# Optimization experiments

Hardware: AMD Instinct MI355X
Metric: run time of the kernel (lower is better)

## Reference

```python
import jax, jax.numpy as jnp
import numpy as np

LT_INDICES = np.array([[0, 1, 3], [1, 2, 4], [3, 4, 5]])  # lower-triangle -> 3x3
SYMEIG_EPS = 1e-6  # noise scale used by SymEig
N_GRADS = 64
B_VALUE = 1000.0


def _design_matrix(n_grads=N_GRADS, b=B_VALUE, seed=0):
    """dipy.reconst.dti.design_matrix equivalent: columns Dxx,Dxy,Dyy,Dxz,Dyz,Dzz, dummy; returns -B."""
    rng = np.random.default_rng(seed)
    g = rng.normal(size=(n_grads, 3))
    g /= np.linalg.norm(g, axis=1, keepdims=True)
    B = np.empty((n_grads, 7), dtype=np.float64)
    B[:, 0] = g[:, 0] * g[:, 0] * b
    B[:, 1] = g[:, 0] * g[:, 1] * 2.0 * b
    B[:, 2] = g[:, 1] * g[:, 1] * b
    B[:, 3] = g[:, 0] * g[:, 2] * 2.0 * b
    B[:, 4] = g[:, 1] * g[:, 2] * 2.0 * b
    B[:, 5] = g[:, 2] * g[:, 2] * b
    B[:, 6] = 1.0
    return -B


def setup_inputs() -> dict:
    key = jax.random.key(0)
    k1, _ = jax.random.split(key)
    D = _design_matrix()
    design_matrix_inv = jnp.asarray(np.linalg.pinv(D), dtype=jnp.float32)  # [7, n_grads]
    min_diffusivity = jnp.asarray(1e-6 / -D.min(), dtype=jnp.float32)
    dwi = jax.random.uniform(k1, (100, 100, 100, N_GRADS), dtype=jnp.float32)
    mask = jnp.ones((100, 100, 100, 1), dtype=jnp.float32)
    return {"dwi": dwi, "mask": mask, "design_matrix_inv": design_matrix_inv,
            "min_diffusivity": min_diffusivity}


def reference(dwi, mask, design_matrix_inv, min_diffusivity):
    # WLS log-linear DTI fit
    dwi = jnp.maximum(dwi, min_diffusivity)
    fit = jnp.einsum('ij,...j->...i', design_matrix_inv, jnp.log(dwi))  # [...,7]
    tensors = fit[..., LT_INDICES]  # [...,3,3] symmetric diffusion tensors
    # SymEig: add tiny gaussian noise (degeneracy breaking), re-symmetrize
    noise = SYMEIG_EPS * jax.random.normal(jax.random.key(42), tensors.shape, dtype=tensors.dtype)
    t = tensors + noise
    t = (t + jnp.swapaxes(t, -1, -2)) * 0.5
    eigenvals, eigenvectors = jnp.linalg.eigh(t)  # [...,3], [...,3,3]
    eigenvals = jnp.maximum(eigenvals, min_diffusivity)
    eigenvals = jnp.where(jnp.isnan(eigenvals), 0.0, eigenvals)
    all_zero = jnp.all(eigenvals == 0, axis=-1).astype(eigenvals.dtype)
    ev1, ev2, ev3 = eigenvals[..., 0], eigenvals[..., 1], eigenvals[..., 2]
    num = 0.5 * ((ev1 - ev2) ** 2 + (ev2 - ev3) ** 2 + (ev3 - ev1) ** 2)
    den = jnp.sum(eigenvals * eigenvals, axis=-1) + all_zero
    fa = jnp.sqrt(num / den)[..., None]  # [...,1]
    return fa * mask
```

## Files before the change

### kernel.cpp

```cpp
#include <hip/hip_runtime.h>


__device__ __forceinline__ unsigned tf_rotl(unsigned x, int r) {
  return (x << r) | (x >> (32 - r));
}

__device__ __forceinline__ unsigned threefry_second(unsigned x0, unsigned x1) {
  const unsigned k0 = 0u, k1 = 42u;
  const unsigned k2 = 0x1BD11BDAu ^ k0 ^ k1;
  x0 += k0; x1 += k1;
#define TF_ROUND(r) { x0 += x1; x1 = tf_rotl(x1, r); x1 ^= x0; }
  TF_ROUND(13) TF_ROUND(15) TF_ROUND(26) TF_ROUND(6)
  x0 += k1; x1 += k2 + 1u;
  TF_ROUND(17) TF_ROUND(29) TF_ROUND(16) TF_ROUND(24)
  x0 += k2; x1 += k0 + 2u;
  TF_ROUND(13) TF_ROUND(15) TF_ROUND(26) TF_ROUND(6)
  x0 += k0; x1 += k1 + 3u;
  TF_ROUND(17) TF_ROUND(29) TF_ROUND(16) TF_ROUND(24)
  x0 += k1; x1 += k2 + 4u;
  TF_ROUND(13) TF_ROUND(15) TF_ROUND(26) TF_ROUND(6)
  x0 += k2; x1 += k0 + 5u;
#undef TF_ROUND
  (void)x0;
  return x1;
}

__device__ __forceinline__ float erfinv_xla(float x) {
  float w = -__logf(fmaf(-x, x, 1.0f));
  float p;
  if (w < 5.0f) {
    w = w - 2.5f;
    p = 2.81022636e-08f;
    p = fmaf(p, w, 3.43273939e-07f);
    p = fmaf(p, w, -3.5233877e-06f);
    p = fmaf(p, w, -4.39150654e-06f);
    p = fmaf(p, w, 0.00021858087f);
    p = fmaf(p, w, -0.00125372503f);
    p = fmaf(p, w, -0.00417768164f);
    p = fmaf(p, w, 0.246640727f);
    p = fmaf(p, w, 1.50140941f);
  } else {
    w = __builtin_sqrtf(w) - 3.0f;
    p = -0.000200214257f;
    p = fmaf(p, w, 0.000100950558f);
    p = fmaf(p, w, 0.00134934322f);
    p = fmaf(p, w, -0.00367342844f);
    p = fmaf(p, w, 0.00573950773f);
    p = fmaf(p, w, -0.0076224613f);
    p = fmaf(p, w, 0.00943887047f);
    p = fmaf(p, w, 1.00167406f);
    p = fmaf(p, w, 2.83297682f);
  }
  return p * x;
}

__device__ __forceinline__ float jax_normal_at(unsigned idx) {
  unsigned bits = threefry_second(0u, idx);
  float f = __uint_as_float((bits >> 9) | 0x3F800000u);
  float u = f - 1.0f;
  const float lo = -0.99999994f;
  float val = fmaf(u, 2.0f, lo);
  val = fmaxf(lo, val);
  return 1.41421356237f * erfinv_xla(val);
}

#define NG 64

__global__ __launch_bounds__(256) void fa_kernel(
    const float* __restrict__ dwi,
    const float* __restrict__ mask,
    const float* __restrict__ W,
    const float* __restrict__ mdp,
    float* __restrict__ out,
    int nvox)
{
  int v = blockIdx.x * 256 + threadIdx.x;
  if (v >= nvox) return;
  const float md = mdp[0];

  const float4* __restrict__ p =
      reinterpret_cast<const float4*>(dwi + (size_t)v * NG);
  float f0 = 0.f, f1 = 0.f, f2 = 0.f, f3 = 0.f, f4 = 0.f, f5 = 0.f;
#pragma unroll
  for (int j4 = 0; j4 < NG / 4; ++j4) {
    float4 d = p[j4];
    float xs[4];
    xs[0] = __logf(fmaxf(d.x, md));
    xs[1] = __logf(fmaxf(d.y, md));
    xs[2] = __logf(fmaxf(d.z, md));
    xs[3] = __logf(fmaxf(d.w, md));
#pragma unroll
    for (int k = 0; k < 4; ++k) {
      int j = j4 * 4 + k;
      float x = xs[k];
      f0 = fmaf(W[0 * NG + j], x, f0);
      f1 = fmaf(W[1 * NG + j], x, f1);
      f2 = fmaf(W[2 * NG + j], x, f2);
      f3 = fmaf(W[3 * NG + j], x, f3);
      f4 = fmaf(W[4 * NG + j], x, f4);
      f5 = fmaf(W[5 * NG + j], x, f5);
    }
  }

  unsigned base = 9u * (unsigned)v;
  float z[9];
#pragma unroll
  for (int e = 0; e < 9; ++e) z[e] = jax_normal_at(base + (unsigned)e);

  const float eps = 1e-6f;
  float a00 = f0 + eps * z[0];
  float a11 = f2 + eps * z[4];
  float a22 = f5 + eps * z[8];
  float a01 = ((f1 + eps * z[1]) + (f1 + eps * z[3])) * 0.5f;
  float a02 = ((f3 + eps * z[2]) + (f3 + eps * z[6])) * 0.5f;
  float a12 = ((f4 + eps * z[5]) + (f4 + eps * z[7])) * 0.5f;

  float q = (a00 + a11 + a22) * (1.0f / 3.0f);
  float aa = a00 - q, bb = a11 - q, cc = a22 - q;
  float p2 = aa * aa + bb * bb + cc * cc +
             2.0f * (a01 * a01 + a02 * a02 + a12 * a12);
  float pp = __builtin_sqrtf(p2 * (1.0f / 6.0f));
  float invp = (pp > 0.0f) ? (1.0f / pp) : 0.0f;
  float b00 = aa * invp, b11 = bb * invp, b22 = cc * invp;
  float b01 = a01 * invp, b02 = a02 * invp, b12 = a12 * invp;
  float detB = b00 * (b11 * b22 - b12 * b12)
             - b01 * (b01 * b22 - b12 * b02)
             + b02 * (b01 * b12 - b11 * b02);
  float r = 0.5f * detB;
  r = fminf(1.0f, fmaxf(-1.0f, r));
  float phi = acosf(r) * (1.0f / 3.0f);
  float l0 = q + 2.0f * pp * cosf(phi);
  float l2 = q + 2.0f * pp * cosf(phi + 2.0943951023931953f);
  float l1 = 3.0f * q - l0 - l2;

  l0 = fmaxf(l0, md);
  l1 = fmaxf(l1, md);
  l2 = fmaxf(l2, md);
  float d01 = l0 - l1, d12 = l1 - l2, d20 = l2 - l0;
  float num = 0.5f * (d01 * d01 + d12 * d12 + d20 * d20);
  float den = l0 * l0 + l1 * l1 + l2 * l2;
  float fa = __builtin_sqrtf(num / den);

  out[v] = fa * mask[v];
}

extern "C" void kernel_launch(void* const* d_in, const int* in_sizes, int n_in,
                              void* d_out, int out_size, void* d_ws, size_t ws_size,
                              hipStream_t stream) {
  const float* dwi  = (const float*)d_in[0];
  const float* mask = (const float*)d_in[1];
  const float* W    = (const float*)d_in[2];
  const float* mdp  = (const float*)d_in[3];
  float* out = (float*)d_out;
  int nvox = in_sizes[0] / NG;
  int grid = (nvox + 255) / 256;
  hipLaunchKernelGGL(fa_kernel, dim3(grid), dim3(256), 0, stream,
                     dwi, mask, W, mdp, out, nvox);
}
```

Before: 357.8 us.

## Stage DWI tile into LDS via global_load_lds with XOR swizzle

Each block now copies its 256 voxels' gradient data into shared memory with coalesced direct global-to-LDS loads. The source slots are XOR-swizzled so that each thread's per-voxel float4 reads from LDS avoid bank conflicts. Previously every thread read its own contiguous 256-byte row with strided float4 loads, which coalesced poorly across the wavefront. The change uses 64 KB of LDS per block, which may limit occupancy, and adds a block-wide barrier before compute.

```diff
diff --git a/kernel.cpp b/kernel.cpp
--- a/kernel.cpp
+++ b/kernel.cpp
@@ -1,4 +1,5 @@
 #include <hip/hip_runtime.h>
+#include <stdint.h>
 
 
 __device__ __forceinline__ unsigned tf_rotl(unsigned x, int r) {
@@ -65,6 +66,10 @@
 }
 
 #define NG 64
+#define VPB 256
+
+typedef __attribute__((address_space(1))) const void gvoid_t;
+typedef __attribute__((address_space(3))) void lvoid_t;
 
 __global__ __launch_bounds__(256) void fa_kernel(
     const float* __restrict__ dwi,
@@ -74,16 +79,40 @@
     float* __restrict__ out,
     int nvox)
 {
-  int v = blockIdx.x * 256 + threadIdx.x;
+  __shared__ float4 smem[VPB * NG / 4];
+
+  const int t    = threadIdx.x;
+  const int wid  = t >> 6;
+  const int lane = t & 63;
+
+  const size_t blockBaseF = (size_t)blockIdx.x * VPB * NG;
+  const float* gbase = dwi + blockBaseF;
+  const size_t validSlots = ((size_t)nvox * NG - blockBaseF) >> 2;
+
+#pragma unroll
+  for (int i = 0; i < 16; ++i) {
+    const int baseSlot = wid * 1024 + i * 64;
+    const int slot = baseSlot + lane;
+    int srcSlot = slot ^ ((slot >> 4) & 7);
+    if ((size_t)srcSlot >= validSlots) srcSlot = 0;
+    __builtin_amdgcn_global_load_lds(
+        (gvoid_t*)(gbase + (size_t)srcSlot * 4),
+        (lvoid_t*)(smem + baseSlot),
+        16, 0, 0);
+  }
+  __syncthreads();
+
+  const int v = blockIdx.x * VPB + t;
   if (v >= nvox) return;
+
   const float md = mdp[0];
 
-  const float4* __restrict__ p =
-      reinterpret_cast<const float4*>(dwi + (size_t)v * NG);
+  const int rb = t << 4;
+  const int sw = t & 7;
   float f0 = 0.f, f1 = 0.f, f2 = 0.f, f3 = 0.f, f4 = 0.f, f5 = 0.f;
 #pragma unroll
-  for (int j4 = 0; j4 < NG / 4; ++j4) {
-    float4 d = p[j4];
+  for (int j4 = 0; j4 < 16; ++j4) {
+    float4 d = smem[rb + (j4 ^ sw)];
     float xs[4];
     xs[0] = __logf(fmaxf(d.x, md));
     xs[1] = __logf(fmaxf(d.y, md));
@@ -153,7 +182,7 @@
   const float* mdp  = (const float*)d_in[3];
   float* out = (float*)d_out;
   int nvox = in_sizes[0] / NG;
-  int grid = (nvox + 255) / 256;
-  hipLaunchKernelGGL(fa_kernel, dim3(grid), dim3(256), 0, stream,
+  int grid = (nvox + VPB - 1) / VPB;
+  hipLaunchKernelGGL(fa_kernel, dim3(grid), dim3(VPB), 0, stream,
                      dwi, mask, W, mdp, out, nvox);
 }
```

Result: slower. 372.6 us (+4.1%).

## Stage DWI through LDS with async global_load_lds double buffering

Applied to the files above, without the earlier changes.

Replaces per-thread strided float4 loads of each voxel's 64 gradients with wave-cooperative global_load_lds transfers into a swizzled, double-buffered shared-memory tile. The loads are issued ahead of the threefry noise generation so memory latency overlaps that compute, and later chunks are prefetched while earlier ones are consumed. The goal is coalesced global access in place of 256-byte-strided per-thread reads, plus overlap of load latency. It depends on manual vmcnt waits and an XOR swizzle being exactly right, adds 32KB of LDS per block, and sets launch_bounds to 4 blocks.

```diff
diff --git a/kernel.cpp b/kernel.cpp
--- a/kernel.cpp
+++ b/kernel.cpp
@@ -1,4 +1,5 @@
 #include <hip/hip_runtime.h>
+#include <stdint.h>
 
 
 __device__ __forceinline__ unsigned tf_rotl(unsigned x, int r) {
@@ -66,7 +67,13 @@
 
 #define NG 64
 
-__global__ __launch_bounds__(256) void fa_kernel(
+typedef __attribute__((address_space(1))) const void gvoid_t;
+typedef __attribute__((address_space(3))) void lvoid_t;
+
+#define VMWAIT(n) asm volatile("s_waitcnt vmcnt(" #n ")" ::: "memory")
+#define CLOB()    asm volatile("" ::: "memory")
+
+__global__ __launch_bounds__(256, 4) void fa_kernel(
     const float* __restrict__ dwi,
     const float* __restrict__ mask,
     const float* __restrict__ W,
@@ -74,38 +81,78 @@
     float* __restrict__ out,
     int nvox)
 {
-  int v = blockIdx.x * 256 + threadIdx.x;
-  if (v >= nvox) return;
+  __shared__ float4 smem[4][2][256];
+
+  const int t    = threadIdx.x;
+  const int wid  = t >> 6;
+  const int lane = t & 63;
+  const int v    = blockIdx.x * 256 + t;
+  const size_t wvox    = (size_t)blockIdx.x * 256 + (size_t)(wid * 64);
+  const size_t totalF4 = (size_t)nvox * (NG / 4);
+
   const float md = mdp[0];
 
-  const float4* __restrict__ p =
-      reinterpret_cast<const float4*>(dwi + (size_t)v * NG);
+#define STAGE(c, b) do {                                                   \
+    _Pragma("unroll")                                                      \
+    for (int i = 0; i < 4; ++i) {                                          \
+      int vl = i * 16 + (lane >> 2);                                       \
+      int q  = (lane & 3) ^ ((vl >> 1) & 3);                               \
+      size_t src = (wvox + (size_t)vl) * (NG / 4) + (c) * 4 + (size_t)q;   \
+      if (src >= totalF4) src = 0;            \
+      __builtin_amdgcn_global_load_lds(                                    \
+          (gvoid_t*)(dwi + src * 4),                                       \
+          (lvoid_t*)(&smem[wid][(b)][i * 64]), 16, 0, 0);                  \
+    }                                                                      \
+    CLOB();                                                                \
+  } while (0)
+
   float f0 = 0.f, f1 = 0.f, f2 = 0.f, f3 = 0.f, f4 = 0.f, f5 = 0.f;
-#pragma unroll
-  for (int j4 = 0; j4 < NG / 4; ++j4) {
-    float4 d = p[j4];
-    float xs[4];
-    xs[0] = __logf(fmaxf(d.x, md));
-    xs[1] = __logf(fmaxf(d.y, md));
-    xs[2] = __logf(fmaxf(d.z, md));
-    xs[3] = __logf(fmaxf(d.w, md));
-#pragma unroll
-    for (int k = 0; k < 4; ++k) {
-      int j = j4 * 4 + k;
-      float x = xs[k];
-      f0 = fmaf(W[0 * NG + j], x, f0);
-      f1 = fmaf(W[1 * NG + j], x, f1);
-      f2 = fmaf(W[2 * NG + j], x, f2);
-      f3 = fmaf(W[3 * NG + j], x, f3);
-      f4 = fmaf(W[4 * NG + j], x, f4);
-      f5 = fmaf(W[5 * NG + j], x, f5);
-    }
-  }
+  const int swz   = (lane >> 1) & 3;
+  const int rbase = lane * 4;
+
+#define MATVEC(c, b) do {                                                  \
+    _Pragma("unroll")                                                      \
+    for (int j = 0; j < 4; ++j) {                                          \
+      float4 d = smem[wid][(b)][rbase + (j ^ swz)];                        \
+      float xs[4];                                                         \
+      xs[0] = __logf(fmaxf(d.x, md));                                      \
+      xs[1] = __logf(fmaxf(d.y, md));                                      \
+      xs[2] = __logf(fmaxf(d.z, md));                                      \
+      xs[3] = __logf(fmaxf(d.w, md));                                      \
+      _Pragma("unroll")                                                    \
+      for (int k = 0; k < 4; ++k) {                                        \
+        int jg = (c) * 16 + j * 4 + k;                                     \
+        float x = xs[k];                                                   \
+        f0 = fmaf(W[0 * NG + jg], x, f0);                                  \
+        f1 = fmaf(W[1 * NG + jg], x, f1);                                  \
+        f2 = fmaf(W[2 * NG + jg], x, f2);                                  \
+        f3 = fmaf(W[3 * NG + jg], x, f3);                                  \
+        f4 = fmaf(W[4 * NG + jg], x, f4);                                  \
+        f5 = fmaf(W[5 * NG + jg], x, f5);                                  \
+      }                                                                    \
+    }                                                                      \
+  } while (0)
+
+  STAGE(0, 0);
+  STAGE(1, 1);
 
   unsigned base = 9u * (unsigned)v;
   float z[9];
 #pragma unroll
   for (int e = 0; e < 9; ++e) z[e] = jax_normal_at(base + (unsigned)e);
+
+  VMWAIT(4);
+  MATVEC(0, 0);
+  STAGE(2, 0);
+  VMWAIT(4);
+  MATVEC(1, 1);
+  STAGE(3, 1);
+  float mv = mask[v < nvox ? v : 0];
+  CLOB();
+  VMWAIT(5);
+  MATVEC(2, 0);
+  VMWAIT(1);
+  MATVEC(3, 1);
 
   const float eps = 1e-6f;
   float a00 = f0 + eps * z[0];
@@ -141,7 +188,7 @@
   float den = l0 * l0 + l1 * l1 + l2 * l2;
   float fa = __builtin_sqrtf(num / den);
 
-  out[v] = fa * mask[v];
+  if (v < nvox) out[v] = fa * mv;
 }
 
 extern "C" void kernel_launch(void* const* d_in, const int* in_sizes, int n_in,
```

Result: no change. 357.2 us (-0.2%).
